# Kernel tuning notes

Hardware: AMD Instinct MI355X
Metric: run time of the kernel (lower is better)

Reference implementation:

```python
import jax, jax.numpy as jnp
import numpy as np
from jax import lax

HEADS, HEAD_DIM, DIM, DIM_OUT, EPS = 12, 64, 768, 768, 1e-5
REL_DIM = 2 * 56 - 1  # 2*max(q_size, kv_size) - 1


def setup_inputs():
    key = jax.random.key(0)
    ks = jax.random.split(key, 10)
    B, T, H, W = 4, 1, 56, 56
    N = 1 + T * H * W
    s = 0.02
    return {
        "x": jax.random.normal(ks[0], (B, N, DIM), jnp.float32),
        "Wqkv": jax.random.normal(ks[1], (DIM, 3 * DIM_OUT), jnp.float32) * s,
        "pool_q_w": jax.random.normal(ks[2], (HEAD_DIM, 1, 3, 3), jnp.float32) * 0.1,
        "pool_k_w": jax.random.normal(ks[3], (HEAD_DIM, 1, 3, 3), jnp.float32) * 0.1,
        "pool_v_w": jax.random.normal(ks[4], (HEAD_DIM, 1, 3, 3), jnp.float32) * 0.1,
        "gq": jnp.ones((HEAD_DIM,), jnp.float32), "bq": jnp.zeros((HEAD_DIM,), jnp.float32),
        "gk": jnp.ones((HEAD_DIM,), jnp.float32), "bk": jnp.zeros((HEAD_DIM,), jnp.float32),
        "gv": jnp.ones((HEAD_DIM,), jnp.float32), "bv": jnp.zeros((HEAD_DIM,), jnp.float32),
        "rel_pos_h": jax.random.normal(ks[5], (REL_DIM, HEAD_DIM), jnp.float32) * s,
        "rel_pos_w": jax.random.normal(ks[6], (REL_DIM, HEAD_DIM), jnp.float32) * s,
        "Wproj": jax.random.normal(ks[7], (DIM_OUT, DIM_OUT), jnp.float32) * s,
        "bproj": jnp.zeros((DIM_OUT,), jnp.float32),
        "T": 1, "H": 56, "W": 56,
    }


def _layernorm(y, g, b):
    mu = y.mean(-1, keepdims=True)
    var = ((y - mu) ** 2).mean(-1, keepdims=True)
    return (y - mu) * lax.rsqrt(var + EPS) * g + b


def _pool(t, w, stride, g, b, B, H, W):
    # t: (B, heads, 1 + H*W, head_dim). Split cls, depthwise conv over spatial body.
    cls, body = t[:, :, :1], t[:, :, 1:]
    y = body.reshape(B * HEADS, H, W, HEAD_DIM).transpose(0, 3, 1, 2)  # (BH, C, H, W)
    y = lax.conv_general_dilated(y, w, (stride, stride), [(1, 1), (1, 1)],
                                 feature_group_count=HEAD_DIM,
                                 dimension_numbers=("NCHW", "OIHW", "NCHW"))
    Ho, Wo = y.shape[2], y.shape[3]
    y = y.reshape(B, HEADS, HEAD_DIM, Ho * Wo).transpose(0, 1, 3, 2)
    y = jnp.concatenate([cls, y], axis=2)
    return _layernorm(y, g, b), Ho, Wo


def _forward(x, Wqkv, pool_q_w, pool_k_w, pool_v_w, gq, bq, gk, bk, gv, bv,
             rel_pos_h, rel_pos_w, Wproj, bproj, T, H, W):
    B, N, _ = x.shape
    scale = HEAD_DIM ** -0.5
    qkv = (x @ Wqkv).reshape(B, N, 3, HEADS, HEAD_DIM).transpose(2, 0, 3, 1, 4)
    q, k, v = qkv[0], qkv[1], qkv[2]  # (B, heads, N, head_dim)
    q, q_h, q_w = _pool(q, pool_q_w, 1, gq, bq, B, H, W)
    k, k_h, k_w = _pool(k, pool_k_w, 2, gk, bk, B, H, W)
    v, _, _ = _pool(v, pool_v_w, 2, gv, bv, B, H, W)
    attn = jnp.einsum("bhqd,bhkd->bhqk", q * scale, k)
    # relative position bias; index tables are static (shapes known at trace time)
    dh = (np.arange(q_h)[:, None] * max(k_h / q_h, 1.0)
          - np.arange(k_h)[None, :] * max(q_h / k_h, 1.0)
          + (k_h - 1) * max(q_h / k_h, 1.0)).astype(np.int32)
    dw = (np.arange(q_w)[:, None] * max(k_w / q_w, 1.0)
          - np.arange(k_w)[None, :] * max(q_w / k_w, 1.0)
          + (k_w - 1) * max(q_w / k_w, 1.0)).astype(np.int32)
    Rh, Rw = rel_pos_h[dh], rel_pos_w[dw]  # (q_h, k_h, c), (q_w, k_w, c)
    r_q = q[:, :, 1:].reshape(B, HEADS, q_h, q_w, HEAD_DIM)
    rel_h = jnp.einsum("byhwc,hkc->byhwk", r_q, Rh)
    rel_w = jnp.einsum("byhwc,wkc->byhwk", r_q, Rw)
    body = (attn[:, :, 1:, 1:].reshape(B, HEADS, q_h, q_w, k_h, k_w)
            + rel_h[..., None] + rel_w[..., None, :])
    attn = attn.at[:, :, 1:, 1:].set(body.reshape(B, HEADS, q_h * q_w, k_h * k_w))
    attn = jax.nn.softmax(attn, axis=-1)
    out = attn @ v
    out = out.at[:, :, 1:, :].add(q[:, :, 1:, :])  # residual pooling (skips cls)
    out = out.transpose(0, 2, 1, 3).reshape(B, -1, DIM_OUT)
    return out @ Wproj + bproj


def reference(x, Wqkv, pool_q_w, pool_k_w, pool_v_w, gq, bq, gk, bk, gv, bv,
              rel_pos_h, rel_pos_w, Wproj, bproj, T, H, W):
    return _forward(x, Wqkv, pool_q_w, pool_k_w, pool_v_w, gq, bq, gk, bk, gv, bv,
                    rel_pos_h, rel_pos_w, Wproj, bproj, T, H, W)
```

## Files before the change

kernel.cpp:

```cpp
#include <hip/hip_runtime.h>
#include <hip/hip_bf16.h>

#define BATCH 4
#define NTOK 3137
#define DIM 768
#define NHEAD 12
#define HD 64
#define QH 56
#define QW 56
#define NKEY 785
#define NKEYPAD 800
#define THREE_DIM 2304
#define MROWS (BATCH*NTOK)
#define QT2 128
#define NQT2 25
#define NBH 48
#define RELROWS (NBH*56)
#define XD 128

#define QSCALE 0.1803368801111204f
#define QUNSCALE 5.5451774444795625f
#define PADSUP  -43.3f

typedef __attribute__((ext_vector_type(8))) short bf16x8;
typedef __attribute__((ext_vector_type(4))) float f32x4;

__device__ __forceinline__ unsigned short f2bf(float f) {
    union { float f; unsigned u; } v; v.f = f;
    unsigned r = v.u + 0x7FFFu + ((v.u >> 16) & 1u);
    return (unsigned short)(r >> 16);
}
__device__ __forceinline__ float bf2f(unsigned short s) {
    union { unsigned u; float f; } v; v.u = (unsigned)s << 16; return v.f;
}

__device__ __forceinline__ void gl16(const void* g, void* l) {
    __builtin_amdgcn_global_load_lds(
        (const __attribute__((address_space(1))) unsigned int*)g,
        (__attribute__((address_space(3))) unsigned int*)l, 16, 0, 0);
}

__global__ __launch_bounds__(256) void cvt_bf16(
    const float* __restrict__ in, unsigned short* __restrict__ outp, int n4)
{
    for (int i = blockIdx.x * 256 + threadIdx.x; i < n4; i += gridDim.x * 256) {
        float4 v = reinterpret_cast<const float4*>(in)[i];
        union { unsigned short s[4]; uint2 u; } o;
        o.s[0] = f2bf(v.x); o.s[1] = f2bf(v.y);
        o.s[2] = f2bf(v.z); o.s[3] = f2bf(v.w);
        reinterpret_cast<uint2*>(outp)[i] = o.u;
    }
}

__global__ __launch_bounds__(256) void cvt_rel(
    const float* __restrict__ h, const float* __restrict__ w,
    unsigned short* __restrict__ hb, unsigned short* __restrict__ wb)
{
    int i = blockIdx.x * 256 + threadIdx.x;
    const float* src; unsigned short* dst; int j;
    if (i < 1776)      { src = h; dst = hb; j = i; }
    else if (i < 3552) { src = w; dst = wb; j = i - 1776; }
    else return;
    float4 v = reinterpret_cast<const float4*>(src)[j];
    union { unsigned short s[4]; uint2 u; } o;
    o.s[0] = f2bf(v.x); o.s[1] = f2bf(v.y);
    o.s[2] = f2bf(v.z); o.s[3] = f2bf(v.w);
    reinterpret_cast<uint2*>(dst)[j] = o.u;
}

__global__ __launch_bounds__(256) void transpose_bf16_2(
    const float* __restrict__ W0, unsigned short* __restrict__ Wt0,
    const float* __restrict__ W1, unsigned short* __restrict__ Wt1)
{
    const float* W; unsigned short* Wt; int N;
    if (blockIdx.z == 0) { W = W0; Wt = Wt0; N = THREE_DIM; }
    else {
        if (blockIdx.x >= DIM / 32) return;
        W = W1; Wt = Wt1; N = DIM;
    }
    const int K = DIM;
    __shared__ float tile[32][33];
    int k0 = blockIdx.y * 32, n0 = blockIdx.x * 32;
    int t = threadIdx.x;
    int r = t >> 5, c = t & 31;
    #pragma unroll
    for (int p = 0; p < 4; ++p)
        tile[r + p * 8][c] = W[(size_t)(k0 + r + p * 8) * N + n0 + c];
    __syncthreads();
    #pragma unroll
    for (int p = 0; p < 4; ++p)
        Wt[(size_t)(n0 + r + p * 8) * K + k0 + c] = f2bf(tile[c][r + p * 8]);
}

__global__ __launch_bounds__(256, 3) void gemm_mfma(
    const unsigned short* __restrict__ A, const unsigned short* __restrict__ Bt,
    const float* __restrict__ bias, void* __restrict__ C,
    int M, int N, int K, int out_bf16)
{
    __shared__ __align__(16) char lds[49152];
    int t = threadIdx.x;
    int wave = t >> 6, lane = t & 63;
    int lm = lane & 15, lkg = lane >> 4;
    int wr = wave >> 1, wc = wave & 1;

    int gx = gridDim.x;
    int nwg = gx * gridDim.y;
    int lin = blockIdx.y * gx + blockIdx.x;
    int qq = nwg >> 3, rr = nwg & 7;
    int xcd = lin & 7, idx = lin >> 3;
    int newlin = (xcd < rr ? xcd * (qq + 1) : rr * (qq + 1) + (xcd - rr) * qq) + idx;
    int m0 = (newlin / gx) * 128, n0 = (newlin % gx) * 128;

    const unsigned short *gpa0, *gpa1, *gpb0, *gpb1;
    int la0, la1, lb0, lb1;
    {
        int o0 = t * 16, o1 = 4096 + t * 16;
        int r0 = o0 >> 6, s0 = ((o0 >> 4) & 3) ^ ((r0 >> 1) & 3);
        int r1 = o1 >> 6, s1 = ((o1 >> 4) & 3) ^ ((r1 >> 1) & 3);
        int ar0 = m0 + r0; if (ar0 >= M) ar0 = M - 1;
        int ar1 = m0 + r1; if (ar1 >= M) ar1 = M - 1;
        gpa0 = A + (size_t)ar0 * K + s0 * 8;  la0 = o0;
        gpa1 = A + (size_t)ar1 * K + s1 * 8;  la1 = o1;
        gpb0 = Bt + (size_t)(n0 + r0) * K + s0 * 8;  lb0 = 8192 + o0;
        gpb1 = Bt + (size_t)(n0 + r1) * K + s1 * 8;  lb1 = 8192 + o1;
    }

    f32x4 acc[4][4] = {};
    const int nt = K >> 5;

    gl16(gpa0, &lds[la0]); gl16(gpa1, &lds[la1]);
    gl16(gpb0, &lds[lb0]); gl16(gpb1, &lds[lb1]);
    gpa0 += 32; gpa1 += 32; gpb0 += 32; gpb1 += 32;
    gl16(gpa0, &lds[16384 + la0]); gl16(gpa1, &lds[16384 + la1]);
    gl16(gpb0, &lds[16384 + lb0]); gl16(gpb1, &lds[16384 + lb1]);
    gpa0 += 32; gpa1 += 32; gpb0 += 32; gpb1 += 32;

    int cur = 0;
    for (int tt = 0; tt < nt; ++tt) {
        if (tt + 1 < nt) asm volatile("s_waitcnt vmcnt(4)" ::: "memory");
        else             asm volatile("s_waitcnt vmcnt(0)" ::: "memory");
        __builtin_amdgcn_s_barrier();

        if (tt + 2 < nt) {
            int nx = cur + 2; if (nx >= 3) nx -= 3;
            char* nb = &lds[nx << 14];
            gl16(gpa0, nb + la0); gl16(gpa1, nb + la1);
            gl16(gpb0, nb + lb0); gl16(gpb1, nb + lb1);
            gpa0 += 32; gpa1 += 32; gpb0 += 32; gpb1 += 32;
        }

        char* base = &lds[cur << 14];
        bf16x8 af[4], bfr[4];
        #pragma unroll
        for (int m = 0; m < 4; ++m) {
            int row = wr * 64 + m * 16 + lm;
            af[m] = *reinterpret_cast<const bf16x8*>(
                base + row * 64 + ((lkg ^ ((row >> 1) & 3)) << 4));
        }
        #pragma unroll
        for (int n = 0; n < 4; ++n) {
            int row = wc * 64 + n * 16 + lm;
            bfr[n] = *reinterpret_cast<const bf16x8*>(
                base + 8192 + row * 64 + ((lkg ^ ((row >> 1) & 3)) << 4));
        }
        __builtin_amdgcn_s_setprio(1);
        #pragma unroll
        for (int m = 0; m < 4; ++m)
            #pragma unroll
            for (int n = 0; n < 4; ++n)
                acc[m][n] = __builtin_amdgcn_mfma_f32_16x16x32_bf16(
                    af[m], bfr[n], acc[m][n], 0, 0, 0);
        __builtin_amdgcn_s_setprio(0);

        cur = (cur == 2) ? 0 : cur + 1;
    }

    float bv[4];
    #pragma unroll
    for (int n = 0; n < 4; ++n)
        bv[n] = bias ? bias[n0 + wc * 64 + n * 16 + lm] : 0.f;
    #pragma unroll
    for (int m = 0; m < 4; ++m) {
        #pragma unroll
        for (int r = 0; r < 4; ++r) {
            int row = m0 + wr * 64 + m * 16 + lkg * 4 + r;
            if (row >= M) continue;
            #pragma unroll
            for (int n = 0; n < 4; ++n) {
                int col = n0 + wc * 64 + n * 16 + lm;
                float o = acc[m][n][r] + bv[n];
                if (out_bf16)
                    ((unsigned short*)C)[(size_t)row * N + col] = f2bf(o);
                else
                    ((float*)C)[(size_t)row * N + col] = o;
            }
        }
    }
}

__device__ __forceinline__ void pool_body(
    const unsigned short* src, const float* w, const float* g,
    const float* beta, unsigned short* outp, int bh, int orow,
    int stride, int OW, int mode, unsigned short* ibuf,
    int t, int wave, int lane)
{
    for (int i = t; i < 3 * 56 * 32; i += 256) {
        int pair = i >> 5, off = i & 31;
        int r = pair / 56, iw = pair % 56;
        int ih = orow * stride + r - 1;
        unsigned v = 0;
        if (ih >= 0 && ih < QH)
            v = *reinterpret_cast<const unsigned*>(
                src + (size_t)(1 + ih * QW + iw) * THREE_DIM + off * 2);
        *reinterpret_cast<unsigned*>(&ibuf[pair * 64 + off * 2]) = v;
    }

    float wreg[9];
    #pragma unroll
    for (int k = 0; k < 9; ++k) wreg[k] = w[lane * 9 + k];
    float gl = g[lane], bl = beta[lane];
    __syncthreads();

    int ntask = OW + ((orow == 0) ? 1 : 0);
    for (int task = wave; task < ntask; task += 4) {
        float val;
        int pos;
        if (task == OW) {
            val = bf2f(src[lane]);
            pos = 0;
        } else {
            int ow = task;
            float acc = 0.f;
            #pragma unroll
            for (int r = 0; r < 3; ++r) {
                #pragma unroll
                for (int c = 0; c < 3; ++c) {
                    int iwc = ow * stride + c - 1;
                    if (iwc < 0 || iwc >= QW) continue;
                    acc += bf2f(ibuf[(r * 56 + iwc) * 64 + lane]) * wreg[r * 3 + c];
                }
            }
            val = acc;
            pos = 1 + orow * OW + ow;
        }

        float mu = val;
        #pragma unroll
        for (int off = 32; off > 0; off >>= 1) mu += __shfl_xor(mu, off, 64);
        mu *= (1.f / 64.f);
        float dv = val - mu;
        float var = dv * dv;
        #pragma unroll
        for (int off = 32; off > 0; off >>= 1) var += __shfl_xor(var, off, 64);
        var *= (1.f / 64.f);
        float o = dv * rsqrtf(var + 1e-5f) * gl + bl;

        if (mode == 3) {
            unsigned short* row = outp + ((size_t)bh * NTOK + pos) * XD;
            row[lane] = f2bf(o * QSCALE);
            row[64 + lane] = (lane == 56) ? f2bf(PADSUP) : 0;
        } else if (mode == 1) {
            unsigned short* row = outp + ((size_t)bh * NKEYPAD + pos) * XD;
            row[lane] = f2bf(o);
            unsigned short ext = 0;
            if (pos > 0) {
                int kh = (pos - 1) / 28, kw = (pos - 1) % 28;
                if ((lane < 28 && lane == kh) ||
                    (lane >= 28 && lane < 56 && lane - 28 == kw))
                    ext = 0x3F80;
            }
            row[64 + lane] = ext;
        } else {
            outp[((size_t)bh * HD + lane) * NKEYPAD + pos] = f2bf(o);
        }
    }
}

__global__ __launch_bounds__(256) void pool_ln_q(
    const unsigned short* __restrict__ qkvb, const float* __restrict__ w,
    const float* __restrict__ g, const float* __restrict__ beta,
    unsigned short* __restrict__ outp)
{
    __shared__ unsigned short ibuf[3 * 56 * 64];
    int bid = blockIdx.x;
    int orow = bid % QH;
    int bh = bid / QH;
    int head = bh % NHEAD, b = bh / NHEAD;
    const unsigned short* src =
        qkvb + (size_t)b * NTOK * THREE_DIM + (size_t)head * HD;
    pool_body(src, w, g, beta, outp, bh, orow, 1, QW, 3, ibuf,
              threadIdx.x, threadIdx.x >> 6, threadIdx.x & 63);
}

__global__ __launch_bounds__(256) void pool_ln_kv(
    const unsigned short* __restrict__ qkvb,
    const float* __restrict__ wk, const float* __restrict__ gk,
    const float* __restrict__ bk, unsigned short* __restrict__ kpx,
    const float* __restrict__ wv, const float* __restrict__ gv,
    const float* __restrict__ bv, unsigned short* __restrict__ vt16)
{
    __shared__ unsigned short ibuf[3 * 56 * 64];
    int bid = blockIdx.x;
    int orow = bid % 28;
    int bh = bid / 28;
    int head = bh % NHEAD, b = bh / NHEAD;
    int isv = blockIdx.y;
    const unsigned short* src = qkvb + (size_t)b * NTOK * THREE_DIM
        + (size_t)(isv ? 2 : 1) * DIM + (size_t)head * HD;
    if (isv)
        pool_body(src, wv, gv, bv, vt16, bh, orow, 2, 28, 2, ibuf,
                  threadIdx.x, threadIdx.x >> 6, threadIdx.x & 63);
    else
        pool_body(src, wk, gk, bk, kpx, bh, orow, 2, 28, 1, ibuf,
                  threadIdx.x, threadIdx.x >> 6, threadIdx.x & 63);
}

__global__ __launch_bounds__(64) void pad_kv(
    unsigned short* __restrict__ kpx, unsigned short* __restrict__ vt16)
{
    int bh = blockIdx.x;
    int t = threadIdx.x;
    for (int pos = NKEY; pos < NKEYPAD; ++pos) {
        unsigned short* row = kpx + ((size_t)bh * NKEYPAD + pos) * XD;
        row[t] = 0;
        row[64 + t] = (t == 56) ? 0x3F80 : 0;
        vt16[((size_t)bh * HD + t) * NKEYPAD + pos] = 0;
    }
}

__global__ __launch_bounds__(256) void rel_mfma(
    const unsigned short* __restrict__ qpx, const unsigned short* __restrict__ rh,
    const unsigned short* __restrict__ rw, unsigned short* __restrict__ qpx_out)
{
    __shared__ char bbuf[4096];
    int X = blockIdx.x;
    int m0 = blockIdx.y * 256;
    int mode = blockIdx.z;
    const unsigned short* rtab = mode ? rw : rh;
    int t = threadIdx.x;
    int wave = t >> 6, lane = t & 63;
    int lm = lane & 15, lkg = lane >> 4;

    {
        int row = t >> 3, c8 = t & 7;
        int4 val = {0, 0, 0, 0};
        if (row < 28) {
            int dh = X - 2 * row + 54;
            val = *reinterpret_cast<const int4*>(rtab + (size_t)dh * HD + c8 * 8);
        }
        *reinterpret_cast<int4*>(&bbuf[row * 128 + ((c8 * 16) ^ ((row & 7) << 4))]) = val;
    }
    __syncthreads();

    int rbase = m0 + wave * 64 + lm;
    f32x4 acc[4][2] = {};
    #pragma unroll
    for (int kc = 0; kc < 2; ++kc) {
        bf16x8 bfrag[2];
        #pragma unroll
        for (int nb = 0; nb < 2; ++nb) {
            int row = nb * 16 + lm;
            bfrag[nb] = *reinterpret_cast<const bf16x8*>(
                &bbuf[row * 128 + (((kc * 4 + lkg) * 16) ^ ((row & 7) << 4))]);
        }
        #pragma unroll
        for (int m = 0; m < 4; ++m) {
            int rho = rbase + m * 16; if (rho > RELROWS - 1) rho = RELROWS - 1;
            int bh = rho / 56, rem = rho % 56;
            int pos1 = (mode == 0) ? X * 56 + rem : rem * 56 + X;
            const unsigned short* qsrc =
                qpx + ((size_t)bh * NTOK + 1 + pos1) * XD + kc * 32 + lkg * 8;
            bf16x8 af = *reinterpret_cast<const bf16x8*>(qsrc);
            acc[m][0] = __builtin_amdgcn_mfma_f32_16x16x32_bf16(af, bfrag[0], acc[m][0], 0, 0, 0);
            acc[m][1] = __builtin_amdgcn_mfma_f32_16x16x32_bf16(af, bfrag[1], acc[m][1], 0, 0, 0);
        }
    }

    #pragma unroll
    for (int m = 0; m < 4; ++m) {
        #pragma unroll
        for (int r = 0; r < 4; ++r) {
            int rho = m0 + wave * 64 + m * 16 + lkg * 4 + r;
            if (rho >= RELROWS) continue;
            int bh = rho / 56, rem = rho % 56;
            int pos1 = (mode == 0) ? X * 56 + rem : rem * 56 + X;
            unsigned short* dst =
                qpx_out + ((size_t)bh * NTOK + 1 + pos1) * XD + 64 + mode * 28;
            dst[lm] = f2bf(acc[m][0][r] * 8.f);
            if (lm < 12) dst[16 + lm] = f2bf(acc[m][1][r] * 8.f);
        }
    }
}

__global__ __launch_bounds__(512, 4) void attn_mfma(
    const unsigned short* __restrict__ qpx, const unsigned short* __restrict__ kpx,
    const unsigned short* __restrict__ vt, unsigned short* __restrict__ outp)
{
    __shared__ __align__(16) char kbuf[3][8192];
    __shared__ __align__(16) char vbuf[3][4096];
    __shared__ __align__(16) char pbuf[8][1024];

    int bid0 = blockIdx.x;
    int bid = (bid0 & 7) * ((NBH * NQT2) / 8) + (bid0 >> 3);
    int tile = bid % NQT2;
    int bh = bid / NQT2;
    int head = bh % NHEAD, b = bh / NHEAD;
    int q0 = tile * QT2;
    int t = threadIdx.x;
    int wave = t >> 6, lane = t & 63;
    int lm = lane & 15, lkg = lane >> 4;

    const unsigned short* kb  = kpx + (size_t)bh * NKEYPAD * XD;
    const unsigned short* vtb = vt + (size_t)bh * HD * NKEYPAD;

    bf16x8 qf[4] = {};
    int qrow = q0 + wave * 16 + lm;
    if (qrow < NTOK) {
        const unsigned short* qs = qpx + ((size_t)bh * NTOK + qrow) * XD + lkg * 8;
        qf[0] = *reinterpret_cast<const bf16x8*>(qs);
        qf[1] = *reinterpret_cast<const bf16x8*>(qs + 32);
        qf[2] = *reinterpret_cast<const bf16x8*>(qs + 64);
        qf[3] = *reinterpret_cast<const bf16x8*>(qs + 96);
    }

    f32x4 oacc[4] = {};
    float osum[4] = {0.f, 0.f, 0.f, 0.f};

    int kr = t >> 4;
    int ks = (t & 15) ^ (kr & 7);
    const unsigned short* kp0 = kb + (size_t)kr * XD + ks * 8;
    int kd = t * 16;
    int vidx = t & 255;
    int vr = vidx >> 2;
    int vs = (vidx & 3) ^ ((vr >> 1) & 3);
    const unsigned short* vp0 = vtb + (size_t)vr * NKEYPAD + vs * 8;
    int vd = vidx * 16;

    const int NT = NKEYPAD / 32;

    int pwa = (lkg << 5) + ((lm >> 3) << 4) + (lm & 7) * 2;
    int pra = ((lm >> 2) << 5) + ((lkg & 1) << 4) + ((lm & 3) << 7) + ((lkg >> 1) << 9);

    gl16(kp0, &kbuf[0][kd]); gl16(vp0, &vbuf[0][vd]);
    kp0 += 32 * XD; vp0 += 32;
    gl16(kp0, &kbuf[1][kd]); gl16(vp0, &vbuf[1][vd]);
    kp0 += 32 * XD; vp0 += 32;

    int cur = 0;
    for (int jt = 0; jt < NT; ++jt) {
        if (jt + 1 < NT) asm volatile("s_waitcnt vmcnt(2)" ::: "memory");
        else             asm volatile("s_waitcnt vmcnt(0)" ::: "memory");
        __builtin_amdgcn_s_barrier();

        if (jt + 2 < NT) {
            int nx = cur + 2; if (nx >= 3) nx -= 3;
            gl16(kp0, &kbuf[nx][kd]);
            gl16(vp0, &vbuf[nx][vd]);
            kp0 += 32 * XD; vp0 += 32;
        }

        f32x4 acc0 = {0.f, 0.f, 0.f, 0.f}, acc1 = {0.f, 0.f, 0.f, 0.f};
        __builtin_amdgcn_s_setprio(1);
        #pragma unroll
        for (int kc = 0; kc < 4; ++kc) {
            int sl = (kc * 4 + lkg) ^ (lm & 7);
            bf16x8 kf0 = *reinterpret_cast<const bf16x8*>(&kbuf[cur][lm * 256 + sl * 16]);
            acc0 = __builtin_amdgcn_mfma_f32_16x16x32_bf16(qf[kc], kf0, acc0, 0, 0, 0);
            bf16x8 kf1 = *reinterpret_cast<const bf16x8*>(&kbuf[cur][(16 + lm) * 256 + sl * 16]);
            acc1 = __builtin_amdgcn_mfma_f32_16x16x32_bf16(qf[kc], kf1, acc1, 0, 0, 0);
        }
        __builtin_amdgcn_s_setprio(0);

        #pragma unroll
        for (int nb = 0; nb < 2; ++nb) {
            f32x4 a = nb ? acc1 : acc0;
            #pragma unroll
            for (int r = 0; r < 4; ++r) {
                float e;
                asm("v_exp_f32 %0, %1" : "=v"(e) : "v"(a[r]));
                osum[r] += e;
                union { float f; unsigned u; } ue; ue.f = e;
                *reinterpret_cast<unsigned short*>(
                    &pbuf[wave][pwa + (r << 7) + (nb << 9)]) =
                    (unsigned short)(ue.u >> 16);
            }
        }

        bf16x8 pf = *reinterpret_cast<const bf16x8*>(&pbuf[wave][pra]);
        __builtin_amdgcn_s_setprio(1);
        #pragma unroll
        for (int db = 0; db < 4; ++db) {
            int row = db * 16 + lm;
            bf16x8 vf = *reinterpret_cast<const bf16x8*>(
                &vbuf[cur][row * 64 + ((lkg ^ ((row >> 1) & 3)) << 4)]);
            oacc[db] = __builtin_amdgcn_mfma_f32_16x16x32_bf16(pf, vf, oacc[db], 0, 0, 0);
        }
        __builtin_amdgcn_s_setprio(0);

        cur = (cur == 2) ? 0 : cur + 1;
    }

    #pragma unroll
    for (int r = 0; r < 4; ++r) {
        float s = osum[r];
        s += __shfl_xor(s, 1, 64);
        s += __shfl_xor(s, 2, 64);
        s += __shfl_xor(s, 4, 64);
        s += __shfl_xor(s, 8, 64);
        osum[r] = 1.f / s;
    }
    #pragma unroll
    for (int r = 0; r < 4; ++r) {
        int qpos = q0 + wave * 16 + lkg * 4 + r;
        if (qpos >= NTOK) continue;
        unsigned short* orow = outp + ((size_t)b * NTOK + qpos) * DIM + (size_t)head * HD;
        const unsigned short* qres = qpx + ((size_t)bh * NTOK + qpos) * XD;
        #pragma unroll
        for (int db = 0; db < 4; ++db) {
            int d = db * 16 + lm;
            float o = oacc[db][r] * osum[r];
            if (qpos > 0) o += bf2f(qres[d]) * QUNSCALE;
            orow[d] = f2bf(o);
        }
    }
}

extern "C" void kernel_launch(void* const* d_in, const int* in_sizes, int n_in,
                              void* d_out, int out_size, void* d_ws, size_t ws_size,
                              hipStream_t stream) {
    const float* x     = (const float*)d_in[0];
    const float* Wqkv  = (const float*)d_in[1];
    const float* pqw   = (const float*)d_in[2];
    const float* pkw   = (const float*)d_in[3];
    const float* pvw   = (const float*)d_in[4];
    const float* gq    = (const float*)d_in[5];
    const float* bq    = (const float*)d_in[6];
    const float* gk    = (const float*)d_in[7];
    const float* bk    = (const float*)d_in[8];
    const float* gv    = (const float*)d_in[9];
    const float* bv    = (const float*)d_in[10];
    const float* rph   = (const float*)d_in[11];
    const float* rpw   = (const float*)d_in[12];
    const float* Wproj = (const float*)d_in[13];
    const float* bproj = (const float*)d_in[14];

    unsigned short* qkvb  = (unsigned short*)d_ws;
    unsigned short* qpx   = qkvb + (size_t)MROWS * THREE_DIM;
    unsigned short* kpx   = qpx + (size_t)NBH * NTOK * XD;
    unsigned short* vt16  = kpx + (size_t)NBH * NKEYPAD * XD;
    unsigned short* xbf   = vt16 + (size_t)NBH * HD * NKEYPAD;
    unsigned short* wqkvt = xbf + (size_t)MROWS * DIM;
    unsigned short* wprojt= wqkvt + (size_t)DIM * THREE_DIM;
    unsigned short* rphb  = wprojt + (size_t)DIM * DIM;
    unsigned short* rpwb  = rphb + 7104;
    unsigned short* attn_bf = qkvb;

    dim3 blk(256);

    cvt_bf16<<<2048, blk, 0, stream>>>(x, xbf, (int)((size_t)MROWS * DIM / 4));
    {
        dim3 g(THREE_DIM / 32, DIM / 32, 2);
        transpose_bf16_2<<<g, blk, 0, stream>>>(Wqkv, wqkvt, Wproj, wprojt);
    }
    cvt_rel<<<14, blk, 0, stream>>>(rph, rpw, rphb, rpwb);

    {
        dim3 grid(THREE_DIM / 128, (MROWS + 127) / 128);
        gemm_mfma<<<grid, blk, 0, stream>>>(xbf, wqkvt, nullptr, qkvb,
                                            MROWS, THREE_DIM, DIM, 1);
    }

    pool_ln_q<<<NBH * QH, blk, 0, stream>>>(qkvb, pqw, gq, bq, qpx);
    {
        dim3 g(NBH * 28, 2);
        pool_ln_kv<<<g, blk, 0, stream>>>(qkvb, pkw, gk, bk, kpx,
                                          pvw, gv, bv, vt16);
    }
    pad_kv<<<NBH, 64, 0, stream>>>(kpx, vt16);

    {
        dim3 g(56, (RELROWS + 255) / 256, 2);
        rel_mfma<<<g, blk, 0, stream>>>(qpx, rphb, rpwb, qpx);
    }

    attn_mfma<<<NBH * NQT2, 512, 0, stream>>>(qpx, kpx, vt16, attn_bf);

    {
        dim3 grid(DIM / 128, (MROWS + 127) / 128);
        gemm_mfma<<<grid, blk, 0, stream>>>(attn_bf, wprojt, bproj, d_out,
                                            MROWS, DIM, DIM, 0);
    }
}
```

Baseline: 278.0 us.

## Process two query row-blocks per wave in attention with transposed QK MFMA

The attention kernel drops from 8 waves of 16 query rows to 4 waves (256 threads) of 32 query rows, so each K/V fragment read from shared memory feeds two row blocks. The QK MFMA operands are swapped so each lane's scores sit along the query row, which lets P be packed and written to LDS as 8-byte stores and read back linearly. Row sums now need only cross-lane-group shuffles. This targets LDS read traffic and the softmax store overhead, at the cost of more registers per wave and fewer waves per block.

```diff
diff --git a/kernel.cpp b/kernel.cpp
--- a/kernel.cpp
+++ b/kernel.cpp
@@ -392,13 +392,13 @@
     }
 }
 
-__global__ __launch_bounds__(512, 4) void attn_mfma(
+__global__ __launch_bounds__(256, 3) void attn_mfma(
     const unsigned short* __restrict__ qpx, const unsigned short* __restrict__ kpx,
     const unsigned short* __restrict__ vt, unsigned short* __restrict__ outp)
 {
     __shared__ __align__(16) char kbuf[3][8192];
     __shared__ __align__(16) char vbuf[3][4096];
-    __shared__ __align__(16) char pbuf[8][1024];
+    __shared__ __align__(16) char pbuf[4][2048];
 
     int bid0 = blockIdx.x;
     int bid = (bid0 & 7) * ((NBH * NQT2) / 8) + (bid0 >> 3);
@@ -413,87 +413,101 @@
     const unsigned short* kb  = kpx + (size_t)bh * NKEYPAD * XD;
     const unsigned short* vtb = vt + (size_t)bh * HD * NKEYPAD;
 
-    bf16x8 qf[4] = {};
-    int qrow = q0 + wave * 16 + lm;
-    if (qrow < NTOK) {
-        const unsigned short* qs = qpx + ((size_t)bh * NTOK + qrow) * XD + lkg * 8;
-        qf[0] = *reinterpret_cast<const bf16x8*>(qs);
-        qf[1] = *reinterpret_cast<const bf16x8*>(qs + 32);
-        qf[2] = *reinterpret_cast<const bf16x8*>(qs + 64);
-        qf[3] = *reinterpret_cast<const bf16x8*>(qs + 96);
-    }
-
-    f32x4 oacc[4] = {};
-    float osum[4] = {0.f, 0.f, 0.f, 0.f};
+    bf16x8 qf[2][4] = {};
+    #pragma unroll
+    for (int rb = 0; rb < 2; ++rb) {
+        int qrow = q0 + wave * 32 + rb * 16 + lm;
+        if (qrow < NTOK) {
+            const unsigned short* qs = qpx + ((size_t)bh * NTOK + qrow) * XD + lkg * 8;
+            qf[rb][0] = *reinterpret_cast<const bf16x8*>(qs);
+            qf[rb][1] = *reinterpret_cast<const bf16x8*>(qs + 32);
+            qf[rb][2] = *reinterpret_cast<const bf16x8*>(qs + 64);
+            qf[rb][3] = *reinterpret_cast<const bf16x8*>(qs + 96);
+        }
+    }
+
+    f32x4 oacc[2][4] = {};
+    float osum[2] = {0.f, 0.f};
 
     int kr = t >> 4;
     int ks = (t & 15) ^ (kr & 7);
     const unsigned short* kp0 = kb + (size_t)kr * XD + ks * 8;
-    int kd = t * 16;
-    int vidx = t & 255;
-    int vr = vidx >> 2;
-    int vs = (vidx & 3) ^ ((vr >> 1) & 3);
+    const unsigned short* kp1 = kb + (size_t)(kr + 16) * XD + ks * 8;
+    int kd0 = t * 16, kd1 = 4096 + t * 16;
+    int vr = t >> 2;
+    int vs = (t & 3) ^ ((vr >> 1) & 3);
     const unsigned short* vp0 = vtb + (size_t)vr * NKEYPAD + vs * 8;
-    int vd = vidx * 16;
+    int vd = t * 16;
 
     const int NT = NKEYPAD / 32;
 
-    int pwa = (lkg << 5) + ((lm >> 3) << 4) + (lm & 7) * 2;
-    int pra = ((lm >> 2) << 5) + ((lkg & 1) << 4) + ((lm & 3) << 7) + ((lkg >> 1) << 9);
-
-    gl16(kp0, &kbuf[0][kd]); gl16(vp0, &vbuf[0][vd]);
-    kp0 += 32 * XD; vp0 += 32;
-    gl16(kp0, &kbuf[1][kd]); gl16(vp0, &vbuf[1][vd]);
-    kp0 += 32 * XD; vp0 += 32;
+    gl16(kp0, &kbuf[0][kd0]); gl16(kp1, &kbuf[0][kd1]); gl16(vp0, &vbuf[0][vd]);
+    kp0 += 32 * XD; kp1 += 32 * XD; vp0 += 32;
+    gl16(kp0, &kbuf[1][kd0]); gl16(kp1, &kbuf[1][kd1]); gl16(vp0, &vbuf[1][vd]);
+    kp0 += 32 * XD; kp1 += 32 * XD; vp0 += 32;
+
+    int pwbase = lm * 16 + ((lkg & 1) << 3);
 
     int cur = 0;
     for (int jt = 0; jt < NT; ++jt) {
-        if (jt + 1 < NT) asm volatile("s_waitcnt vmcnt(2)" ::: "memory");
+        if (jt + 1 < NT) asm volatile("s_waitcnt vmcnt(3)" ::: "memory");
         else             asm volatile("s_waitcnt vmcnt(0)" ::: "memory");
         __builtin_amdgcn_s_barrier();
 
         if (jt + 2 < NT) {
             int nx = cur + 2; if (nx >= 3) nx -= 3;
-            gl16(kp0, &kbuf[nx][kd]);
+            gl16(kp0, &kbuf[nx][kd0]);
+            gl16(kp1, &kbuf[nx][kd1]);
             gl16(vp0, &vbuf[nx][vd]);
-            kp0 += 32 * XD; vp0 += 32;
-        }
-
-        f32x4 acc0 = {0.f, 0.f, 0.f, 0.f}, acc1 = {0.f, 0.f, 0.f, 0.f};
+            kp0 += 32 * XD; kp1 += 32 * XD; vp0 += 32;
+        }
+
+        f32x4 a00 = {0.f,0.f,0.f,0.f}, a01 = {0.f,0.f,0.f,0.f};
+        f32x4 a10 = {0.f,0.f,0.f,0.f}, a11 = {0.f,0.f,0.f,0.f};
         __builtin_amdgcn_s_setprio(1);
         #pragma unroll
         for (int kc = 0; kc < 4; ++kc) {
             int sl = (kc * 4 + lkg) ^ (lm & 7);
             bf16x8 kf0 = *reinterpret_cast<const bf16x8*>(&kbuf[cur][lm * 256 + sl * 16]);
-            acc0 = __builtin_amdgcn_mfma_f32_16x16x32_bf16(qf[kc], kf0, acc0, 0, 0, 0);
             bf16x8 kf1 = *reinterpret_cast<const bf16x8*>(&kbuf[cur][(16 + lm) * 256 + sl * 16]);
-            acc1 = __builtin_amdgcn_mfma_f32_16x16x32_bf16(qf[kc], kf1, acc1, 0, 0, 0);
+            a00 = __builtin_amdgcn_mfma_f32_16x16x32_bf16(kf0, qf[0][kc], a00, 0, 0, 0);
+            a01 = __builtin_amdgcn_mfma_f32_16x16x32_bf16(kf1, qf[0][kc], a01, 0, 0, 0);
+            a10 = __builtin_amdgcn_mfma_f32_16x16x32_bf16(kf0, qf[1][kc], a10, 0, 0, 0);
+            a11 = __builtin_amdgcn_mfma_f32_16x16x32_bf16(kf1, qf[1][kc], a11, 0, 0, 0);
         }
         __builtin_amdgcn_s_setprio(0);
 
         #pragma unroll
-        for (int nb = 0; nb < 2; ++nb) {
-            f32x4 a = nb ? acc1 : acc0;
+        for (int rb = 0; rb < 2; ++rb) {
             #pragma unroll
-            for (int r = 0; r < 4; ++r) {
-                float e;
-                asm("v_exp_f32 %0, %1" : "=v"(e) : "v"(a[r]));
-                osum[r] += e;
-                union { float f; unsigned u; } ue; ue.f = e;
-                *reinterpret_cast<unsigned short*>(
-                    &pbuf[wave][pwa + (r << 7) + (nb << 9)]) =
-                    (unsigned short)(ue.u >> 16);
+            for (int nb = 0; nb < 2; ++nb) {
+                f32x4 a = rb ? (nb ? a11 : a10) : (nb ? a01 : a00);
+                float e0, e1, e2, e3;
+                asm("v_exp_f32 %0, %1" : "=v"(e0) : "v"(a[0]));
+                asm("v_exp_f32 %0, %1" : "=v"(e1) : "v"(a[1]));
+                asm("v_exp_f32 %0, %1" : "=v"(e2) : "v"(a[2]));
+                asm("v_exp_f32 %0, %1" : "=v"(e3) : "v"(a[3]));
+                osum[rb] += (e0 + e1) + (e2 + e3);
+                union { float f; unsigned u; } u0, u1, u2, u3;
+                u0.f = e0; u1.f = e1; u2.f = e2; u3.f = e3;
+                uint2 pk;
+                pk.x = (u0.u >> 16) | (u1.u & 0xFFFF0000u);
+                pk.y = (u2.u >> 16) | (u3.u & 0xFFFF0000u);
+                int addr = (rb << 10) + ((nb * 2 + (lkg >> 1)) << 8) + pwbase;
+                *reinterpret_cast<uint2*>(&pbuf[wave][addr]) = pk;
             }
         }
 
-        bf16x8 pf = *reinterpret_cast<const bf16x8*>(&pbuf[wave][pra]);
+        bf16x8 pf0 = *reinterpret_cast<const bf16x8*>(&pbuf[wave][lane * 16]);
+        bf16x8 pf1 = *reinterpret_cast<const bf16x8*>(&pbuf[wave][1024 + lane * 16]);
         __builtin_amdgcn_s_setprio(1);
         #pragma unroll
         for (int db = 0; db < 4; ++db) {
             int row = db * 16 + lm;
             bf16x8 vf = *reinterpret_cast<const bf16x8*>(
                 &vbuf[cur][row * 64 + ((lkg ^ ((row >> 1) & 3)) << 4)]);
-            oacc[db] = __builtin_amdgcn_mfma_f32_16x16x32_bf16(pf, vf, oacc[db], 0, 0, 0);
+            oacc[0][db] = __builtin_amdgcn_mfma_f32_16x16x32_bf16(pf0, vf, oacc[0][db], 0, 0, 0);
+            oacc[1][db] = __builtin_amdgcn_mfma_f32_16x16x32_bf16(pf1, vf, oacc[1][db], 0, 0, 0);
         }
         __builtin_amdgcn_s_setprio(0);
 
@@ -501,26 +515,27 @@
     }
 
     #pragma unroll
-    for (int r = 0; r < 4; ++r) {
-        float s = osum[r];
-        s += __shfl_xor(s, 1, 64);
-        s += __shfl_xor(s, 2, 64);
-        s += __shfl_xor(s, 4, 64);
-        s += __shfl_xor(s, 8, 64);
-        osum[r] = 1.f / s;
-    }
-    #pragma unroll
-    for (int r = 0; r < 4; ++r) {
-        int qpos = q0 + wave * 16 + lkg * 4 + r;
-        if (qpos >= NTOK) continue;
-        unsigned short* orow = outp + ((size_t)b * NTOK + qpos) * DIM + (size_t)head * HD;
-        const unsigned short* qres = qpx + ((size_t)bh * NTOK + qpos) * XD;
-        #pragma unroll
-        for (int db = 0; db < 4; ++db) {
-            int d = db * 16 + lm;
-            float o = oacc[db][r] * osum[r];
-            if (qpos > 0) o += bf2f(qres[d]) * QUNSCALE;
-            orow[d] = f2bf(o);
+    for (int rb = 0; rb < 2; ++rb) {
+        osum[rb] += __shfl_xor(osum[rb], 16, 64);
+        osum[rb] += __shfl_xor(osum[rb], 32, 64);
+    }
+    float inv[2] = { 1.f / osum[0], 1.f / osum[1] };
+    #pragma unroll
+    for (int rb = 0; rb < 2; ++rb) {
+        #pragma unroll
+        for (int r = 0; r < 4; ++r) {
+            float invq = __shfl(inv[rb], lkg * 4 + r, 64);
+            int qpos = q0 + wave * 32 + rb * 16 + lkg * 4 + r;
+            if (qpos >= NTOK) continue;
+            unsigned short* orow = outp + ((size_t)b * NTOK + qpos) * DIM + (size_t)head * HD;
+            const unsigned short* qres = qpx + ((size_t)bh * NTOK + qpos) * XD;
+            #pragma unroll
+            for (int db = 0; db < 4; ++db) {
+                int d = db * 16 + lm;
+                float o = oacc[rb][db][r] * invq;
+                if (qpos > 0) o += bf2f(qres[d]) * QUNSCALE;
+                orow[d] = f2bf(o);
+            }
         }
     }
 }
@@ -583,7 +598,7 @@
         rel_mfma<<<g, blk, 0, stream>>>(qpx, rphb, rpwb, qpx);
     }
 
-    attn_mfma<<<NBH * NQT2, 512, 0, stream>>>(qpx, kpx, vt16, attn_bf);
+    attn_mfma<<<NBH * NQT2, blk, 0, stream>>>(qpx, kpx, vt16, attn_bf);
 
     {
         dim3 grid(DIM / 128, (MROWS + 127) / 128);
```

Result: no change. 276.8 us (median of 2 runs) (-0.4%).
